# Optimization experiments

Measured on AMD Instinct MI355X. Metric: run time of the kernel, lower is better.

The kernel has to match this reference:

```python
import jax, jax.numpy as jnp
import numpy as np

B, C, Himg, Wimg = 8, 256, 128, 128
KC, VC, HID = 256, 256, 1024


def _conv(x, w, b, pad, groups=1):
    y = jax.lax.conv_general_dilated(
        x, w, (1, 1), [(pad[0], pad[0]), (pad[1], pad[1])],
        dimension_numbers=('NCHW', 'OIHW', 'NCHW'), feature_group_count=groups)
    return y + b[None, :, None, None]


def _ln(x, g, b, eps=1e-5):
    m = x.mean(-1, keepdims=True)
    v = ((x - m) ** 2).mean(-1, keepdims=True)
    return (x - m) / jnp.sqrt(v + eps) * g + b


def setup_inputs() -> dict:
    key = jax.random.key(0)
    ks = jax.random.split(key, 24)
    s = 0.02
    inp = {
        'x': jax.random.normal(ks[0], (B, C, Himg, Wimg), jnp.float32),
        'H': Himg, 'W': Wimg,
        # directional K/Q convs: dir0 kernel (1,3), dir1 kernel (3,1)
        'wk1': s * jax.random.normal(ks[1], (KC, C, 1, 3), jnp.float32),
        'bk1': jnp.zeros((KC,), jnp.float32),
        'wk2': s * jax.random.normal(ks[2], (KC, C, 3, 1), jnp.float32),
        'bk2': jnp.zeros((KC,), jnp.float32),
        'wq1': s * jax.random.normal(ks[3], (KC, C, 1, 3), jnp.float32),
        'bq1': jnp.zeros((KC,), jnp.float32),
        'wq2': s * jax.random.normal(ks[4], (KC, C, 3, 1), jnp.float32),
        'bq2': jnp.zeros((KC,), jnp.float32),
        'wv': s * jax.random.normal(ks[5], (VC, C, 1, 1), jnp.float32),
        'bv': jnp.zeros((VC,), jnp.float32),
        'wr': s * jax.random.normal(ks[6], (C, 2 * VC, 1, 1), jnp.float32),
        'br': jnp.zeros((C,), jnp.float32),
        'g1': jnp.ones((C,), jnp.float32), 'b1': jnp.zeros((C,), jnp.float32),
        'g2': jnp.ones((C,), jnp.float32), 'b2': jnp.zeros((C,), jnp.float32),
        'w_fc1': s * jax.random.normal(ks[7], (HID, C), jnp.float32),
        'b_fc1': jnp.zeros((HID,), jnp.float32),
        'w_dw': s * jax.random.normal(ks[8], (HID, 1, 3, 3), jnp.float32),
        'b_dw': jnp.zeros((HID,), jnp.float32),
        'w_fc2': s * jax.random.normal(ks[9], (C, HID), jnp.float32),
        'b_fc2': jnp.zeros((C,), jnp.float32),
    }
    return inp


def reference(x, H, W, wk1, bk1, wk2, bk2, wq1, bq1, wq2, bq2, wv, bv, wr, br,
              g1, b1, g2, b2, w_fc1, b_fc1, w_dw, b_dw, w_fc2, b_fc2):
    b, c, h, w = x.shape
    N = h * w
    xseq = x.reshape(b, c, N).transpose(0, 2, 1)          # b N c
    n1 = _ln(xseq, g1, b1)
    xn = n1.transpose(0, 2, 1).reshape(b, c, h, w)

    val = _conv(xn, wv, bv, (0, 0)).reshape(b, VC, N)     # b vc n
    attended, maps = [], []
    ctx = None
    for (wk, bk, wq, bq, pad) in [(wk1, bk1, wq1, bq1, (0, 1)),
                                  (wk2, bk2, wq2, bq2, (1, 0))]:
        k = _conv(xn, wk, bk, pad).reshape(b, KC, N)
        q = _conv(xn, wq, bq, pad).reshape(b, KC, N)
        key_s = jax.nn.softmax(k, axis=2)                 # softmax over spatial
        qry_s = jax.nn.softmax(q, axis=1)                 # softmax over channels
        ctx = jnp.einsum('bkn,bvn->bkv', key_s, val)      # O(n) linear attention
        av = jnp.einsum('bkv,bkn->bvn', ctx, qry_s).reshape(b, VC, h, w)
        attended.append(av)
        maps.append(key_s.mean(axis=1).reshape(b, h, w))
    agg = jnp.concatenate(attended, axis=1)               # b 2vc h w
    attn = _conv(agg, wr, br, (0, 0))                     # b c h w
    amap = jnp.stack(maps, axis=0).mean(axis=0)

    tx = xseq + attn.reshape(b, c, N).transpose(0, 2, 1)  # residual
    n2 = _ln(tx, g2, b2)
    h1 = n2 @ w_fc1.T + b_fc1                             # b N 4c
    h1img = h1.transpose(0, 2, 1).reshape(b, HID, h, w)
    dw = _conv(h1img, w_dw, b_dw, (1, 1), groups=HID)
    a = jax.nn.gelu(dw.reshape(b, HID, N).transpose(0, 2, 1), approximate=False)
    ffn = a @ w_fc2.T + b_fc2
    mx = (tx + ffn).transpose(0, 2, 1).reshape(b, c, h, w)
    return (mx, ctx, amap)
```

## Files before the change

### kernel.cpp

```cpp
#include <hip/hip_runtime.h>
#include <hip/hip_bf16.h>

#define B_ 8
#define C_ 256
#define H_ 128
#define W_ 128
#define N_ 16384
#define KC_ 256
#define VC_ 256
#define HID_ 1024

typedef unsigned short ushort_t;
typedef __bf16 bf16x8 __attribute__((ext_vector_type(8)));
typedef float f32x4 __attribute__((ext_vector_type(4)));
typedef ushort_t u16x8 __attribute__((ext_vector_type(8)));

static __device__ __forceinline__ ushort_t f2bu(float f) {
  __hip_bfloat16 h = __float2bfloat16(f);
  return *reinterpret_cast<ushort_t*>(&h);
}
static __device__ __forceinline__ float bu2f(ushort_t u) {
  __hip_bfloat16 h;
  *reinterpret_cast<ushort_t*>(&h) = u;
  return __bfloat162float(h);
}

#define GLD16(gp, lp) __builtin_amdgcn_global_load_lds( \
    (const __attribute__((address_space(1))) void*)(gp), \
    (__attribute__((address_space(3))) void*)(lp), 16, 0, 0)

__global__ __launch_bounds__(256) void pack_all(
    const float* __restrict__ wk1, const float* __restrict__ wk2,
    const float* __restrict__ wq1, const float* __restrict__ wq2,
    const float* __restrict__ wv, const float* __restrict__ wfc1,
    const float* __restrict__ wfc2, const float* __restrict__ wdw,
    const float* __restrict__ bk1, const float* __restrict__ bk2,
    const float* __restrict__ bq1, const float* __restrict__ bq2,
    const float* __restrict__ bv, const float* __restrict__ wr,
    ushort_t* __restrict__ zbuf,
    float* __restrict__ bKV, float* __restrict__ bQ, float* __restrict__ wdwT,
    ushort_t* __restrict__ wvp, ushort_t* __restrict__ wfc1p,
    ushort_t* __restrict__ wfc2p, ushort_t* __restrict__ wrp,
    ushort_t* __restrict__ wkkp, ushort_t* __restrict__ wqqp) {
  int idx = blockIdx.x * 256 + threadIdx.x;
  const int MC = KC_ * C_;
  if (idx < 512) {
    zbuf[idx] = 0;
    bQ[idx] = (idx < 256) ? bq1[idx] : bq2[idx - 256];
    return;
  }
  idx -= 512;
  if (idx < 768) {
    bKV[idx] = (idx < 256) ? bk1[idx] : (idx < 512 ? bk2[idx - 256] : bv[idx - 512]);
    return;
  }
  idx -= 768;
  if (idx < 9216) { int c = idx / 9, t = idx % 9; wdwT[t * HID_ + c] = wdw[idx]; return; }
  idx -= 9216;
  if (idx < VC_ * C_) { wvp[idx] = f2bu(wv[idx]); return; }
  idx -= VC_ * C_;
  if (idx < HID_ * C_) { wfc1p[idx] = f2bu(wfc1[idx]); return; }
  idx -= HID_ * C_;
  if (idx < C_ * HID_) { wfc2p[idx] = f2bu(wfc2[idx]); return; }
  idx -= C_ * HID_;
  if (idx < C_ * 512) { wrp[idx] = f2bu(wr[idx]); return; }
  idx -= C_ * 512;
  if (idx < MC) {
    #pragma unroll
    for (int t = 0; t < 3; ++t) wkkp[t * MC + idx] = f2bu(wk1[idx * 3 + t]);
    return;
  }
  idx -= MC;
  if (idx < MC) {
    #pragma unroll
    for (int t = 0; t < 3; ++t) wkkp[3 * MC + t * MC + idx] = f2bu(wk2[idx * 3 + t]);
    return;
  }
  idx -= MC;
  if (idx < MC) {
    #pragma unroll
    for (int t = 0; t < 3; ++t) wqqp[t * MC + idx] = f2bu(wq1[idx * 3 + t]);
    return;
  }
  idx -= MC;
  if (idx < MC) {
    #pragma unroll
    for (int t = 0; t < 3; ++t) wqqp[3 * MC + t * MC + idx] = f2bu(wq2[idx * 3 + t]);
    return;
  }
}

__global__ __launch_bounds__(256) void ln1t_kernel(const float* __restrict__ x,
    const float* __restrict__ g, const float* __restrict__ beta,
    ushort_t* __restrict__ out) {
  __shared__ float T[256][67];
  __shared__ float st[2][4][64];
  __shared__ float mr[64], rs[64];
  int z = blockIdx.z;
  int n0 = blockIdx.x * 64;
  int t = threadIdx.x;
  const float* xb = x + (size_t)z * C_ * N_;
  #pragma unroll
  for (int j = 0; j < 16; ++j) {
    int e = (j * 256 + t) * 4;
    int c = e >> 6, n = e & 63;
    float4 v = *(const float4*)&xb[(size_t)c * N_ + n0 + n];
    T[c][n] = v.x; T[c][n + 1] = v.y; T[c][n + 2] = v.z; T[c][n + 3] = v.w;
  }
  __syncthreads();
  {
    int n = t & 63, part = t >> 6;
    float s1 = 0.f, s2 = 0.f;
    for (int c = part * 64; c < part * 64 + 64; ++c) { float v = T[c][n]; s1 += v; s2 += v * v; }
    st[0][part][n] = s1; st[1][part][n] = s2;
  }
  __syncthreads();
  if (t < 64) {
    float s1 = st[0][0][t] + st[0][1][t] + st[0][2][t] + st[0][3][t];
    float s2 = st[1][0][t] + st[1][1][t] + st[1][2][t] + st[1][3][t];
    float m = s1 * (1.f / C_);
    float v = s2 * (1.f / C_) - m * m;
    mr[t] = m; rs[t] = rsqrtf(v + 1e-5f);
  }
  __syncthreads();
  {
    int n = t >> 2, cc = (t & 3) * 64;
    float m = mr[n], r = rs[n];
    ushort_t* po = out + (size_t)z * N_ * C_ + (size_t)(n0 + n) * C_ + cc;
    #pragma unroll
    for (int j0 = 0; j0 < 64; j0 += 8) {
      u16x8 o;
      #pragma unroll
      for (int j = 0; j < 8; ++j) {
        int c = cc + j0 + j;
        o[j] = f2bu((T[c][n] - m) * r * g[c] + beta[c]);
      }
      *(u16x8*)(po + j0) = o;
    }
  }
}

__global__ __launch_bounds__(256) void ln2t_kernel(const ushort_t* __restrict__ x,
    const float* __restrict__ g, const float* __restrict__ beta,
    ushort_t* __restrict__ out) {
  __shared__ ushort_t T[256][72];
  __shared__ float st[2][4][64];
  __shared__ float mr[64], rs[64];
  int z = blockIdx.z;
  int n0 = blockIdx.x * 64;
  int t = threadIdx.x;
  const ushort_t* xb = x + (size_t)z * C_ * N_;
  #pragma unroll
  for (int j = 0; j < 8; ++j) {
    int e = (j * 256 + t) * 8;
    int c = e >> 6, n = e & 63;
    *(u16x8*)&T[c][n] = *(const u16x8*)&xb[(size_t)c * N_ + n0 + n];
  }
  __syncthreads();
  {
    int n = t & 63, part = t >> 6;
    float s1 = 0.f, s2 = 0.f;
    for (int c = part * 64; c < part * 64 + 64; ++c) { float v = bu2f(T[c][n]); s1 += v; s2 += v * v; }
    st[0][part][n] = s1; st[1][part][n] = s2;
  }
  __syncthreads();
  if (t < 64) {
    float s1 = st[0][0][t] + st[0][1][t] + st[0][2][t] + st[0][3][t];
    float s2 = st[1][0][t] + st[1][1][t] + st[1][2][t] + st[1][3][t];
    float m = s1 * (1.f / C_);
    float v = s2 * (1.f / C_) - m * m;
    mr[t] = m; rs[t] = rsqrtf(v + 1e-5f);
  }
  __syncthreads();
  {
    int n = t >> 2, cc = (t & 3) * 64;
    float m = mr[n], r = rs[n];
    ushort_t* po = out + (size_t)z * N_ * C_ + (size_t)(n0 + n) * C_ + cc;
    #pragma unroll
    for (int j0 = 0; j0 < 64; j0 += 8) {
      u16x8 o;
      #pragma unroll
      for (int j = 0; j < 8; ++j) {
        int c = cc + j0 + j;
        o[j] = f2bu((bu2f(T[c][n]) - m) * r * g[c] + beta[c]);
      }
      *(u16x8*)(po + j0) = o;
    }
  }
}

template<int TAPS, int DIMSEL, int OMODE, int SPLIT, bool BDUAL>
__global__ __launch_bounds__(256) void mfma_gemm(
    const ushort_t* __restrict__ A, long Abatch, int lda, long Aplane, long Adirstride,
    const ushort_t* __restrict__ B, const ushort_t* __restrict__ B2, long Bbatch, int ldb,
    const float* __restrict__ bias,
    const float* __restrict__ resF, const ushort_t* __restrict__ resB, long Resbatch,
    float* __restrict__ outF, ushort_t* __restrict__ outB, ushort_t* __restrict__ outB2,
    ushort_t* __restrict__ outB3,
    long Outbatch, int ldo, int Ksteps, const ushort_t* __restrict__ zbuf) {
  __shared__ ushort_t sm[17408];
  int tid = threadIdx.x;
  int bx = blockIdx.x, by = blockIdx.y, bz = blockIdx.z;
  if (gridDim.x == 128) bx = ((bx & 7) << 4) | (bx >> 3);
  int b = bz / SPLIT, sK = bz % SPLIT;
  long koff = (long)sK * Ksteps * 64;
  int dsel = (DIMSEL == 3) ? (by < 2 ? 1 : 2)
           : (DIMSEL == 4) ? (by < 2 ? 1 : (by < 4 ? 2 : 0))
           : DIMSEL;
  int m0 = (DIMSEL == 3 || DIMSEL == 4) ? ((by & 1) * 128) : (by * 128);
  int bofs = (DIMSEL == 3 || DIMSEL == 4) ? ((by >> 1) * 256) : 0;
  const ushort_t* Ab = A + (size_t)b * Abatch + koff
      + ((DIMSEL == 3 || DIMSEL == 4) ? (long)(by >> 1) * Adirstride : 0L);
  const ushort_t* Bb = B + (size_t)b * Bbatch + (BDUAL ? 0 : koff);
  const ushort_t* B2b = BDUAL ? (B2 + (size_t)b * Bbatch) : nullptr;
  int n0 = bx * 128;
  int lane = tid & 63, wid = tid >> 6, wm = wid >> 1, wn = wid & 1;

  f32x4 acc[4][4];
  #pragma unroll
  for (int i = 0; i < 4; i++)
    #pragma unroll
    for (int j = 0; j < 4; j++) acc[i][j] = (f32x4)0.f;

  for (int t = 0; t < TAPS; ++t) {
    if (TAPS == 3 && dsel == 2) {
      if ((bx == 0 && t == 0) || (bx == H_ - 1 && t == 2)) continue;
    }
    if (DIMSEL == 4 && dsel == 0 && t != 1) continue;
    const ushort_t* At = Ab + ((DIMSEL == 4 && dsel == 0) ? 0L : (long)t * Aplane);
    for (int ks = 0; ks < Ksteps; ++ks) {
      int k0 = ks * 64;
      #pragma unroll
      for (int i = 0; i < 4; i++) {
        int s = tid + i * 256;
        int row = s >> 3, pc = s & 7;
        int lc = pc ^ (row & 7);
        const ushort_t* g = At + (long)(m0 + row) * lda + k0 + lc * 8;
        GLD16(g, &sm[s * 8]);
      }
      #pragma unroll
      for (int i = 0; i < 4; i++) {
        int s = tid + i * 256;
        int row = s >> 3, pc = s & 7;
        int lc = pc ^ (row & 7);
        const ushort_t* g;
        if (BDUAL) {
          const ushort_t* Bsel = (ks < Ksteps / 2) ? Bb : B2b;
          int kb = ((ks < Ksteps / 2) ? ks : ks - Ksteps / 2) * 64;
          g = Bsel + (long)(n0 + row) * ldb + kb + lc * 8;
        } else if (TAPS == 3 && dsel == 1) {
          int wpos = row + (t - 1);
          if (0 <= wpos && wpos < W_)
            g = Bb + (long)(n0 + row + (t - 1)) * ldb + k0 + lc * 8;
          else
            g = zbuf;
        } else if (TAPS == 3 && dsel == 2) {
          g = Bb + (long)(n0 + row + (t - 1) * W_) * ldb + k0 + lc * 8;
        } else {
          g = Bb + (long)(n0 + row) * ldb + k0 + lc * 8;
        }
        GLD16(g, &sm[8192 + s * 8]);
      }
      __syncthreads();
      #pragma unroll
      for (int kk = 0; kk < 2; kk++) {
        bf16x8 av[4], bv[4];
        int r16 = lane & 15;
        int sl = (lane >> 4) + kk * 4;
        #pragma unroll
        for (int fm = 0; fm < 4; fm++) {
          int row = wm * 64 + fm * 16 + r16;
          av[fm] = *(const bf16x8*)&sm[row * 64 + ((sl ^ (row & 7)) * 8)];
        }
        #pragma unroll
        for (int fn = 0; fn < 4; fn++) {
          int row = wn * 64 + fn * 16 + r16;
          bv[fn] = *(const bf16x8*)&sm[8192 + row * 64 + ((sl ^ (row & 7)) * 8)];
        }
        #pragma unroll
        for (int fm = 0; fm < 4; fm++)
          #pragma unroll
          for (int fn = 0; fn < 4; fn++)
            acc[fm][fn] = __builtin_amdgcn_mfma_f32_16x16x32_bf16(av[fm], bv[fn], acc[fm][fn], 0, 0, 0);
      }
      __syncthreads();
    }
  }

  int r16 = lane & 15, rq = lane >> 4;
  if (OMODE == 1 || OMODE == 2 || OMODE == 7) {
    ushort_t* obase;
    if (DIMSEL == 3 || DIMSEL == 4)
      obase = (blockIdx.y >= 4) ? outB3 : (blockIdx.y >= 2 ? outB2 : outB);
    else
      obase = outB;
    ushort_t* ob = obase + (size_t)bz * Outbatch;
    #pragma unroll
    for (int fm = 0; fm < 4; fm++) {
      #pragma unroll
      for (int fn = 0; fn < 4; fn++) {
        int lm = wm * 64 + fm * 16 + rq * 4;
        int ln = wn * 64 + fn * 16 + r16;
        f32x4 a = acc[fm][fn];
        if (OMODE == 2) {
          #pragma unroll
          for (int r = 0; r < 4; r++)
            sm[ln * 136 + lm + r] = f2bu(a[r] + bias[bofs + m0 + lm + r]);
        } else {
          #pragma unroll
          for (int r = 0; r < 4; r++)
            sm[(lm + r) * 136 + ln] = f2bu(a[r] + bias[bofs + m0 + lm + r]);
        }
      }
    }
    __syncthreads();
    int row = tid >> 1, half = (tid & 1) * 64;
    const ushort_t* src = &sm[row * 136 + half];
    if (OMODE == 7) {
      const float* xb = resF + (size_t)bz * Resbatch + (size_t)(m0 + row) * ldo + n0 + half;
      ushort_t* dst = &ob[(size_t)(m0 + row) * ldo + n0 + half];
      #pragma unroll
      for (int j = 0; j < 8; j++) {
        u16x8 v = *(const u16x8*)(src + j * 8);
        float4 x0 = *(const float4*)(xb + j * 8);
        float4 x1 = *(const float4*)(xb + j * 8 + 4);
        u16x8 o;
        o[0] = f2bu(bu2f(v[0]) + x0.x); o[1] = f2bu(bu2f(v[1]) + x0.y);
        o[2] = f2bu(bu2f(v[2]) + x0.z); o[3] = f2bu(bu2f(v[3]) + x0.w);
        o[4] = f2bu(bu2f(v[4]) + x1.x); o[5] = f2bu(bu2f(v[5]) + x1.y);
        o[6] = f2bu(bu2f(v[6]) + x1.z); o[7] = f2bu(bu2f(v[7]) + x1.w);
        *(u16x8*)(dst + j * 8) = o;
      }
    } else {
      ushort_t* dst;
      if (OMODE == 1) dst = &ob[(size_t)(m0 + row) * ldo + n0 + half];
      else            dst = &ob[(size_t)(n0 + row) * ldo + m0 + half];
      #pragma unroll
      for (int j = 0; j < 8; j++)
        *(u16x8*)(dst + j * 8) = *(const u16x8*)(src + j * 8);
    }
  } else {
    #pragma unroll
    for (int fm = 0; fm < 4; fm++) {
      #pragma unroll
      for (int fn = 0; fn < 4; fn++) {
        int mrow = m0 + wm * 64 + fm * 16 + rq * 4;
        int ncol = n0 + wn * 64 + fn * 16 + r16;
        f32x4 a = acc[fm][fn];
        if (OMODE == 6) {
          float* of = outF + (size_t)bz * Outbatch;
          #pragma unroll
          for (int r = 0; r < 4; r++)
            of[(size_t)(mrow + r) * ldo + ncol] = a[r];
        } else if (OMODE == 8) {
          float* of = outF + (size_t)bz * Outbatch;
          const ushort_t* rp = resB + (size_t)bz * Resbatch;
          #pragma unroll
          for (int r = 0; r < 4; r++) {
            size_t o = (size_t)(mrow + r) * ldo + ncol;
            of[o] = a[r] + bias[mrow + r] + bu2f(rp[o]);
          }
        }
      }
    }
  }
}

__global__ __launch_bounds__(256) void softmax_spatial2(ushort_t* __restrict__ p0,
                                                        ushort_t* __restrict__ p1) {
  int r = blockIdx.x;
  ushort_t* p = (r < B_ * KC_) ? (p0 + (size_t)r * N_) : (p1 + (size_t)(r - B_ * KC_) * N_);
  int tid = threadIdx.x;
  __shared__ float red[256];
  u16x8 v[8];
  #pragma unroll
  for (int j = 0; j < 8; j++) v[j] = *(const u16x8*)&p[tid * 8 + j * 2048];
  float mx = -1e30f;
  #pragma unroll
  for (int j = 0; j < 8; j++)
    #pragma unroll
    for (int e = 0; e < 8; e++) mx = fmaxf(mx, bu2f(v[j][e]));
  red[tid] = mx; __syncthreads();
  for (int s = 128; s > 0; s >>= 1) { if (tid < s) red[tid] = fmaxf(red[tid], red[tid + s]); __syncthreads(); }
  mx = red[0]; __syncthreads();
  float sum = 0.f;
  #pragma unroll
  for (int j = 0; j < 8; j++)
    #pragma unroll
    for (int e = 0; e < 8; e++) sum += __expf(bu2f(v[j][e]) - mx);
  red[tid] = sum; __syncthreads();
  for (int s = 128; s > 0; s >>= 1) { if (tid < s) red[tid] += red[tid + s]; __syncthreads(); }
  float inv = 1.f / red[0];
  #pragma unroll
  for (int j = 0; j < 8; j++) {
    u16x8 o;
    #pragma unroll
    for (int e = 0; e < 8; e++) o[e] = f2bu(__expf(bu2f(v[j][e]) - mx) * inv);
    *(u16x8*)&p[tid * 8 + j * 2048] = o;
  }
}

__global__ __launch_bounds__(256) void softmax_channel2(ushort_t* __restrict__ p0,
                                                        ushort_t* __restrict__ p1) {
  int tid = threadIdx.x;
  size_t rowg = (size_t)blockIdx.x * 32 + (tid >> 3);
  int part = tid & 7;
  ushort_t* q = (rowg < (size_t)B_ * N_) ? (p0 + rowg * KC_)
                                         : (p1 + (rowg - (size_t)B_ * N_) * KC_);
  u16x8 v[4];
  #pragma unroll
  for (int j = 0; j < 4; j++) v[j] = *(const u16x8*)&q[part * 8 + j * 64];
  float mx = -1e30f;
  #pragma unroll
  for (int j = 0; j < 4; j++)
    #pragma unroll
    for (int e = 0; e < 8; e++) mx = fmaxf(mx, bu2f(v[j][e]));
  mx = fmaxf(mx, __shfl_xor(mx, 1));
  mx = fmaxf(mx, __shfl_xor(mx, 2));
  mx = fmaxf(mx, __shfl_xor(mx, 4));
  float sum = 0.f;
  #pragma unroll
  for (int j = 0; j < 4; j++)
    #pragma unroll
    for (int e = 0; e < 8; e++) sum += __expf(bu2f(v[j][e]) - mx);
  sum += __shfl_xor(sum, 1);
  sum += __shfl_xor(sum, 2);
  sum += __shfl_xor(sum, 4);
  float inv = 1.f / sum;
  #pragma unroll
  for (int j = 0; j < 4; j++) {
    u16x8 o;
    #pragma unroll
    for (int e = 0; e < 8; e++) o[e] = f2bu(__expf(bu2f(v[j][e]) - mx) * inv);
    *(u16x8*)&q[part * 8 + j * 64] = o;
  }
}

__global__ __launch_bounds__(256) void amap2_kernel(const ushort_t* __restrict__ k0,
    const ushort_t* __restrict__ k1, float* __restrict__ amap) {
  __shared__ float red[256][8];
  int tid = threadIdx.x;
  int ngrp = tid & 63, part = tid >> 6;
  int nblock = blockIdx.x * 512;
  int b = nblock >> 14;
  int n = (nblock & 16383) + ngrp * 8;
  const ushort_t* b0 = k0 + (size_t)b * KC_ * N_ + n;
  const ushort_t* b1 = k1 + (size_t)b * KC_ * N_ + n;
  float s[8];
  #pragma unroll
  for (int j = 0; j < 8; j++) s[j] = 0.f;
  for (int c = part * 64; c < part * 64 + 64; ++c) {
    u16x8 a = *(const u16x8*)&b0[(size_t)c * N_];
    u16x8 d = *(const u16x8*)&b1[(size_t)c * N_];
    #pragma unroll
    for (int j = 0; j < 8; j++) s[j] += bu2f(a[j]) + bu2f(d[j]);
  }
  #pragma unroll
  for (int j = 0; j < 8; j++) red[tid][j] = s[j];
  __syncthreads();
  if (tid < 64) {
    float t[8];
    #pragma unroll
    for (int j = 0; j < 8; j++)
      t[j] = (red[tid][j] + red[tid + 64][j] + red[tid + 128][j] + red[tid + 192][j])
             * (1.f / (2.f * KC_));
    float* dst = amap + (size_t)nblock + tid * 8;
    *(float4*)dst = make_float4(t[0], t[1], t[2], t[3]);
    *(float4*)(dst + 4) = make_float4(t[4], t[5], t[6], t[7]);
  }
}

template<bool F32OUT>
__global__ __launch_bounds__(256) void ctx_reduce(const float* __restrict__ part,
                                                  float* __restrict__ outF,
                                                  ushort_t* __restrict__ outB, int split) {
  int idx = blockIdx.x * 256 + threadIdx.x;
  int b = idx >> 16;
  int r = idx & 65535;
  float s = 0.f;
  for (int k = 0; k < split; k++)
    s += part[((size_t)(b * split + k)) * KC_ * VC_ + r];
  if (F32OUT) outF[idx] = s;
  outB[idx] = f2bu(s);
}

__global__ __launch_bounds__(256) void dwgelu_t(const ushort_t* __restrict__ h1t,
    const float* __restrict__ wdwT, const float* __restrict__ bdw,
    ushort_t* __restrict__ actT) {
  int pix = blockIdx.x * 2 + (threadIdx.x >> 7);
  int c = (threadIdx.x & 127) * 8;
  int h = pix >> 7, w = pix & 127;
  float s[8];
  {
    float4 b0 = *(const float4*)&bdw[c];
    float4 b1 = *(const float4*)&bdw[c + 4];
    s[0]=b0.x; s[1]=b0.y; s[2]=b0.z; s[3]=b0.w;
    s[4]=b1.x; s[5]=b1.y; s[6]=b1.z; s[7]=b1.w;
  }
  #pragma unroll
  for (int di = -1; di <= 1; ++di) {
    int h2 = h + di;
    if ((unsigned)h2 >= H_) continue;
    #pragma unroll
    for (int dj = -1; dj <= 1; ++dj) {
      int w2 = w + dj;
      if ((unsigned)w2 >= W_) continue;
      int tap = (di + 1) * 3 + (dj + 1);
      u16x8 v = *(const u16x8*)&h1t[(size_t)(h2 * W_ + w2) * HID_ + c];
      const float* wp = &wdwT[tap * HID_ + c];
      float4 w0 = *(const float4*)wp, w1 = *(const float4*)(wp + 4);
      s[0] += w0.x * bu2f(v[0]); s[1] += w0.y * bu2f(v[1]);
      s[2] += w0.z * bu2f(v[2]); s[3] += w0.w * bu2f(v[3]);
      s[4] += w1.x * bu2f(v[4]); s[5] += w1.y * bu2f(v[5]);
      s[6] += w1.z * bu2f(v[6]); s[7] += w1.w * bu2f(v[7]);
    }
  }
  u16x8 o;
  #pragma unroll
  for (int j = 0; j < 8; j++) {
    float gl = 0.5f * s[j] * (1.f + erff(s[j] * 0.70710678118654752f));
    o[j] = f2bu(gl);
  }
  *(u16x8*)&actT[(size_t)pix * HID_ + c] = o;
}

extern "C" void kernel_launch(void* const* d_in, const int* in_sizes, int n_in,
                              void* d_out, int out_size, void* d_ws, size_t ws_size,
                              hipStream_t stream) {
  const float* x    = (const float*)d_in[0];
  const float* wk1  = (const float*)d_in[3];
  const float* bk1  = (const float*)d_in[4];
  const float* wk2  = (const float*)d_in[5];
  const float* bk2  = (const float*)d_in[6];
  const float* wq1  = (const float*)d_in[7];
  const float* bq1  = (const float*)d_in[8];
  const float* wq2  = (const float*)d_in[9];
  const float* bq2  = (const float*)d_in[10];
  const float* wv   = (const float*)d_in[11];
  const float* bv   = (const float*)d_in[12];
  const float* wr   = (const float*)d_in[13];
  const float* br   = (const float*)d_in[14];
  const float* g1   = (const float*)d_in[15];
  const float* b1   = (const float*)d_in[16];
  const float* g2   = (const float*)d_in[17];
  const float* b2   = (const float*)d_in[18];
  const float* wfc1 = (const float*)d_in[19];
  const float* bfc1 = (const float*)d_in[20];
  const float* wdw  = (const float*)d_in[21];
  const float* bdw  = (const float*)d_in[22];
  const float* wfc2 = (const float*)d_in[23];
  const float* bfc2 = (const float*)d_in[24];

  const size_t big = (size_t)B_ * C_ * N_;
  const long  CN  = (long)C_ * N_;
  const long  NC2 = (long)N_ * C_;
  const int   MC  = KC_ * C_;

  uint8_t* w8 = (uint8_t*)d_ws;
  size_t off = 0;
  ushort_t* xnt  = (ushort_t*)(w8 + off); off += 67108864;
  ushort_t* kq   = (ushort_t*)(w8 + off); off += 67108864;
  ushort_t* Mbuf = (ushort_t*)(w8 + off); off += (size_t)B_ * C_ * 512 * 2;
  ushort_t* wkkp = (ushort_t*)(w8 + off); off += 6 * MC * 2;
  ushort_t* wvp  = (ushort_t*)(w8 + off); off += MC * 2;
  ushort_t* wqqp = (ushort_t*)(w8 + off); off += 6 * MC * 2;
  ushort_t* wfc1p= (ushort_t*)(w8 + off); off += HID_ * C_ * 2;
  ushort_t* wfc2p= (ushort_t*)(w8 + off); off += C_ * HID_ * 2;
  float* wdwT    = (float*)(w8 + off);    off += 9 * HID_ * 4;
  float* bKV     = (float*)(w8 + off);    off += 768 * 4;
  float* bQ      = (float*)(w8 + off);    off += 512 * 4;
  ushort_t* wrp  = (ushort_t*)(w8 + off); off += C_ * 512 * 2;
  ushort_t* ctx0b= (ushort_t*)(w8 + off); off += (size_t)B_ * KC_ * VC_ * 2;
  ushort_t* ctx1b= (ushort_t*)(w8 + off); off += (size_t)B_ * KC_ * VC_ * 2;
  ushort_t* zbuf = (ushort_t*)(w8 + off); off += 1024;
  float* part    = (float*)(w8 + off);
  size_t need4 = off + (size_t)4 * B_ * KC_ * VC_ * 4;
  size_t need8 = off + (size_t)8 * B_ * KC_ * VC_ * 4;
  int csplit;
  if (ws_size >= need8) csplit = 8;
  else if (ws_size >= need4) csplit = 4;
  else return;
  const float* fzero = (const float*)zbuf;

  float* mx_out   = (float*)d_out;
  float* ctx_out  = mx_out + big;
  float* amap_out = ctx_out + (size_t)B_ * KC_ * VC_;

  ushort_t* mxlo = (ushort_t*)d_out;
  ushort_t* mxhi = (ushort_t*)d_out + big;

  ushort_t* txn  = xnt;
  ushort_t* h1t  = kq;
  ushort_t* actT = kq + (size_t)N_ * HID_;

  dim3 blk(256);

  pack_all<<<3881, blk, 0, stream>>>(wk1, wk2, wq1, wq2, wv, wfc1, wfc2, wdw,
                                     bk1, bk2, bq1, bq2, bv, wr,
                                     zbuf, bKV, bQ, wdwT,
                                     wvp, wfc1p, wfc2p, wrp, wkkp, wqqp);

  ln1t_kernel<<<dim3(N_ / 64, 1, B_), blk, 0, stream>>>(x, g1, b1, xnt);

  mfma_gemm<3, 4, 1, 1, false><<<dim3(N_ / 128, 6, B_), blk, 0, stream>>>(
      wkkp, 0, C_, (long)MC, (long)3 * MC, xnt, nullptr, NC2, C_,
      bKV, nullptr, nullptr, 0,
      nullptr, kq, mxhi, mxlo, (long)KC_ * N_, N_, C_ / 64, zbuf);

  softmax_spatial2<<<2 * B_ * KC_, blk, 0, stream>>>(kq, mxhi);
  amap2_kernel<<<B_ * N_ / 512, blk, 0, stream>>>(kq, mxhi, amap_out);

  for (int d = 0; d < 2; ++d) {
    const ushort_t* Ksrc = d ? mxhi : kq;
    if (csplit == 8)
      mfma_gemm<1, 0, 6, 8, false><<<dim3(VC_ / 128, KC_ / 128, B_ * 8), blk, 0, stream>>>(
          Ksrc, (long)KC_ * N_, N_, 0, 0, mxlo, nullptr, (long)VC_ * N_, N_,
          nullptr, nullptr, nullptr, 0,
          part, nullptr, nullptr, nullptr, (long)KC_ * VC_, VC_, (N_ / 8) / 64, zbuf);
    else
      mfma_gemm<1, 0, 6, 4, false><<<dim3(VC_ / 128, KC_ / 128, B_ * 4), blk, 0, stream>>>(
          Ksrc, (long)KC_ * N_, N_, 0, 0, mxlo, nullptr, (long)VC_ * N_, N_,
          nullptr, nullptr, nullptr, 0,
          part, nullptr, nullptr, nullptr, (long)KC_ * VC_, VC_, (N_ / 4) / 64, zbuf);
    if (d == 0)
      ctx_reduce<false><<<B_ * KC_ * VC_ / 256, blk, 0, stream>>>(part, nullptr, ctx0b, csplit);
    else
      ctx_reduce<true><<<B_ * KC_ * VC_ / 256, blk, 0, stream>>>(part, ctx_out, ctx1b, csplit);
  }

  mfma_gemm<3, 3, 2, 1, false><<<dim3(N_ / 128, 4, B_), blk, 0, stream>>>(
      wqqp, 0, C_, (long)MC, (long)3 * MC, xnt, nullptr, NC2, C_,
      bQ, nullptr, nullptr, 0,
      nullptr, kq, mxlo, nullptr, (long)N_ * KC_, KC_, C_ / 64, zbuf);

  softmax_channel2<<<2 * B_ * N_ / 32, blk, 0, stream>>>(kq, mxlo);

  mfma_gemm<1, 0, 1, 1, false><<<dim3(KC_ / 128, C_ / 128, B_), blk, 0, stream>>>(
      wrp, 0, 512, 0, 0, ctx0b, nullptr, (long)KC_ * VC_, VC_, fzero, nullptr, nullptr, 0,
      nullptr, Mbuf, nullptr, nullptr, (long)C_ * 512, 512, VC_ / 64, zbuf);
  mfma_gemm<1, 0, 1, 1, false><<<dim3(KC_ / 128, C_ / 128, B_), blk, 0, stream>>>(
      wrp + 256, 0, 512, 0, 0, ctx1b, nullptr, (long)KC_ * VC_, VC_, fzero, nullptr, nullptr, 0,
      nullptr, Mbuf + 256, nullptr, nullptr, (long)C_ * 512, 512, VC_ / 64, zbuf);

  mfma_gemm<1, 0, 7, 1, true><<<dim3(N_ / 128, C_ / 128, B_), blk, 0, stream>>>(
      Mbuf, (long)C_ * 512, 512, 0, 0, kq, mxlo, (long)N_ * KC_, KC_,
      br, x, nullptr, CN,
      nullptr, mxhi, nullptr, nullptr, CN, N_, 8, zbuf);

  ln2t_kernel<<<dim3(N_ / 64, 1, B_), blk, 0, stream>>>(mxhi, g2, b2, txn);

  hipMemcpyAsync(part, mxhi + (size_t)7 * CN, (size_t)CN * 2,
                 hipMemcpyDeviceToDevice, stream);

  for (int b = 0; b < B_; ++b) {
    mfma_gemm<1, 0, 2, 1, false><<<dim3(N_ / 128, HID_ / 128, 1), blk, 0, stream>>>(
        wfc1p, 0, C_, 0, 0, txn + (size_t)b * NC2, nullptr, 0, C_,
        bfc1, nullptr, nullptr, 0,
        nullptr, h1t, nullptr, nullptr, 0, HID_, C_ / 64, zbuf);
    dwgelu_t<<<N_ / 2, blk, 0, stream>>>(h1t, wdwT, bdw, actT);
    const ushort_t* txb = (b == 7) ? (const ushort_t*)part : (mxhi + (size_t)b * CN);
    mfma_gemm<1, 0, 8, 1, false><<<dim3(N_ / 128, C_ / 128, 1), blk, 0, stream>>>(
        wfc2p, 0, HID_, 0, 0, actT, nullptr, 0, HID_,
        bfc2, nullptr, txb, 0,
        mx_out + (size_t)b * CN, nullptr, nullptr, nullptr, 0, N_, HID_ / 64, zbuf);
  }
}
```

Measured before the change: 1.437 ms.

## Fuse channel softmax into the output GEMM loader and batch FFN in pairs

The channel softmax pass no longer rewrites the query tensor. A stats kernel stores a per-row max and inverse sum, and the residual GEMM applies exp-normalize while staging B tiles into shared memory. This removes one full read-write pass over the Q tensors, but the B loads become synchronous register loads with extra exp work instead of direct async copies. Separately, when the workspace is large enough, the FFN runs two batches per launch using an extra 64MB activation buffer, halving the launch count and doubling grid size for the FFN kernels.

```diff
diff --git a/kernel.cpp b/kernel.cpp
--- a/kernel.cpp
+++ b/kernel.cpp
@@ -189,7 +189,7 @@
   }
 }
 
-template<int TAPS, int DIMSEL, int OMODE, int SPLIT, bool BDUAL>
+template<int TAPS, int DIMSEL, int OMODE, int SPLIT, bool BDUAL, bool BSOFT>
 __global__ __launch_bounds__(256) void mfma_gemm(
     const ushort_t* __restrict__ A, long Abatch, int lda, long Aplane, long Adirstride,
     const ushort_t* __restrict__ B, const ushort_t* __restrict__ B2, long Bbatch, int ldb,
@@ -197,7 +197,8 @@
     const float* __restrict__ resF, const ushort_t* __restrict__ resB, long Resbatch,
     float* __restrict__ outF, ushort_t* __restrict__ outB, ushort_t* __restrict__ outB2,
     ushort_t* __restrict__ outB3,
-    long Outbatch, int ldo, int Ksteps, const ushort_t* __restrict__ zbuf) {
+    long Outbatch, int ldo, int Ksteps, const ushort_t* __restrict__ zbuf,
+    const float2* __restrict__ qstats) {
   __shared__ ushort_t sm[17408];
   int tid = threadIdx.x;
   int bx = blockIdx.x, by = blockIdx.y, bz = blockIdx.z;
@@ -238,28 +239,47 @@
         const ushort_t* g = At + (long)(m0 + row) * lda + k0 + lc * 8;
         GLD16(g, &sm[s * 8]);
       }
-      #pragma unroll
-      for (int i = 0; i < 4; i++) {
-        int s = tid + i * 256;
-        int row = s >> 3, pc = s & 7;
-        int lc = pc ^ (row & 7);
-        const ushort_t* g;
-        if (BDUAL) {
-          const ushort_t* Bsel = (ks < Ksteps / 2) ? Bb : B2b;
-          int kb = ((ks < Ksteps / 2) ? ks : ks - Ksteps / 2) * 64;
-          g = Bsel + (long)(n0 + row) * ldb + kb + lc * 8;
-        } else if (TAPS == 3 && dsel == 1) {
-          int wpos = row + (t - 1);
-          if (0 <= wpos && wpos < W_)
-            g = Bb + (long)(n0 + row + (t - 1)) * ldb + k0 + lc * 8;
-          else
-            g = zbuf;
-        } else if (TAPS == 3 && dsel == 2) {
-          g = Bb + (long)(n0 + row + (t - 1) * W_) * ldb + k0 + lc * 8;
-        } else {
-          g = Bb + (long)(n0 + row) * ldb + k0 + lc * 8;
+      if (BDUAL && BSOFT) {
+        int dir = (ks < Ksteps / 2) ? 0 : 1;
+        const ushort_t* Bsel = dir ? B2b : Bb;
+        int kb = (ks - dir * (Ksteps / 2)) * 64;
+        #pragma unroll
+        for (int i = 0; i < 4; i++) {
+          int s = tid + i * 256;
+          int row = s >> 3, pc = s & 7;
+          int lc = pc ^ (row & 7);
+          u16x8 e = *(const u16x8*)(Bsel + (long)(n0 + row) * ldb + kb + lc * 8);
+          float2 st = qstats[(size_t)dir * B_ * N_ + (size_t)bz * N_ + n0 + row];
+          u16x8 o;
+          #pragma unroll
+          for (int j = 0; j < 8; j++)
+            o[j] = f2bu(__expf(bu2f(e[j]) - st.x) * st.y);
+          *(u16x8*)&sm[8192 + s * 8] = o;
         }
-        GLD16(g, &sm[8192 + s * 8]);
+      } else {
+        #pragma unroll
+        for (int i = 0; i < 4; i++) {
+          int s = tid + i * 256;
+          int row = s >> 3, pc = s & 7;
+          int lc = pc ^ (row & 7);
+          const ushort_t* g;
+          if (BDUAL) {
+            const ushort_t* Bsel = (ks < Ksteps / 2) ? Bb : B2b;
+            int kb = ((ks < Ksteps / 2) ? ks : ks - Ksteps / 2) * 64;
+            g = Bsel + (long)(n0 + row) * ldb + kb + lc * 8;
+          } else if (TAPS == 3 && dsel == 1) {
+            int wpos = row + (t - 1);
+            if (0 <= wpos && wpos < W_)
+              g = Bb + (long)(n0 + row + (t - 1)) * ldb + k0 + lc * 8;
+            else
+              g = zbuf;
+          } else if (TAPS == 3 && dsel == 2) {
+            g = Bb + (long)(n0 + row + (t - 1) * W_) * ldb + k0 + lc * 8;
+          } else {
+            g = Bb + (long)(n0 + row) * ldb + k0 + lc * 8;
+          }
+          GLD16(g, &sm[8192 + s * 8]);
+        }
       }
       __syncthreads();
       #pragma unroll
@@ -400,13 +420,14 @@
   }
 }
 
-__global__ __launch_bounds__(256) void softmax_channel2(ushort_t* __restrict__ p0,
-                                                        ushort_t* __restrict__ p1) {
+__global__ __launch_bounds__(256) void chstats_kernel(const ushort_t* __restrict__ p0,
+                                                      const ushort_t* __restrict__ p1,
+                                                      float2* __restrict__ qstats) {
   int tid = threadIdx.x;
   size_t rowg = (size_t)blockIdx.x * 32 + (tid >> 3);
   int part = tid & 7;
-  ushort_t* q = (rowg < (size_t)B_ * N_) ? (p0 + rowg * KC_)
-                                         : (p1 + (rowg - (size_t)B_ * N_) * KC_);
+  const ushort_t* q = (rowg < (size_t)B_ * N_) ? (p0 + rowg * KC_)
+                                               : (p1 + (rowg - (size_t)B_ * N_) * KC_);
   u16x8 v[4];
   #pragma unroll
   for (int j = 0; j < 4; j++) v[j] = *(const u16x8*)&q[part * 8 + j * 64];
@@ -426,14 +447,7 @@
   sum += __shfl_xor(sum, 1);
   sum += __shfl_xor(sum, 2);
   sum += __shfl_xor(sum, 4);
-  float inv = 1.f / sum;
-  #pragma unroll
-  for (int j = 0; j < 4; j++) {
-    u16x8 o;
-    #pragma unroll
-    for (int e = 0; e < 8; e++) o[e] = f2bu(__expf(bu2f(v[j][e]) - mx) * inv);
-    *(u16x8*)&q[part * 8 + j * 64] = o;
-  }
+  if (part == 0) qstats[rowg] = make_float2(mx, 1.f / sum);
 }
 
 __global__ __launch_bounds__(256) void amap2_kernel(const ushort_t* __restrict__ k0,
@@ -487,6 +501,8 @@
 __global__ __launch_bounds__(256) void dwgelu_t(const ushort_t* __restrict__ h1t,
     const float* __restrict__ wdwT, const float* __restrict__ bdw,
     ushort_t* __restrict__ actT) {
+  const ushort_t* h1 = h1t + (size_t)blockIdx.y * N_ * HID_;
+  ushort_t* act = actT + (size_t)blockIdx.y * N_ * HID_;
   int pix = blockIdx.x * 2 + (threadIdx.x >> 7);
   int c = (threadIdx.x & 127) * 8;
   int h = pix >> 7, w = pix & 127;
@@ -506,7 +522,7 @@
       int w2 = w + dj;
       if ((unsigned)w2 >= W_) continue;
       int tap = (di + 1) * 3 + (dj + 1);
-      u16x8 v = *(const u16x8*)&h1t[(size_t)(h2 * W_ + w2) * HID_ + c];
+      u16x8 v = *(const u16x8*)&h1[(size_t)(h2 * W_ + w2) * HID_ + c];
       const float* wp = &wdwT[tap * HID_ + c];
       float4 w0 = *(const float4*)wp, w1 = *(const float4*)(wp + 4);
       s[0] += w0.x * bu2f(v[0]); s[1] += w0.y * bu2f(v[1]);
@@ -521,7 +537,7 @@
     float gl = 0.5f * s[j] * (1.f + erff(s[j] * 0.70710678118654752f));
     o[j] = f2bu(gl);
   }
-  *(u16x8*)&actT[(size_t)pix * HID_ + c] = o;
+  *(u16x8*)&act[(size_t)pix * HID_ + c] = o;
 }
 
 extern "C" void kernel_launch(void* const* d_in, const int* in_sizes, int n_in,
@@ -554,6 +570,7 @@
   const size_t big = (size_t)B_ * C_ * N_;
   const long  CN  = (long)C_ * N_;
   const long  NC2 = (long)N_ * C_;
+  const long  NH  = (long)N_ * HID_;
   const int   MC  = KC_ * C_;
 
   uint8_t* w8 = (uint8_t*)d_ws;
@@ -572,14 +589,24 @@
   ushort_t* wrp  = (ushort_t*)(w8 + off); off += C_ * 512 * 2;
   ushort_t* ctx0b= (ushort_t*)(w8 + off); off += (size_t)B_ * KC_ * VC_ * 2;
   ushort_t* ctx1b= (ushort_t*)(w8 + off); off += (size_t)B_ * KC_ * VC_ * 2;
+  float2* qstats = (float2*)(w8 + off);   off += (size_t)2 * B_ * N_ * 8;
   ushort_t* zbuf = (ushort_t*)(w8 + off); off += 1024;
-  float* part    = (float*)(w8 + off);
-  size_t need4 = off + (size_t)4 * B_ * KC_ * VC_ * 4;
-  size_t need8 = off + (size_t)8 * B_ * KC_ * VC_ * 4;
-  int csplit;
-  if (ws_size >= need8) csplit = 8;
-  else if (ws_size >= need4) csplit = 4;
-  else return;
+  const size_t partBytes = (size_t)8 * B_ * KC_ * VC_ * 4;
+  size_t need_pair = off + 67108864 + partBytes;
+  size_t need8 = off + partBytes;
+  size_t need4 = off + partBytes / 2;
+  int csplit; bool pairFFN = false;
+  ushort_t* actX = nullptr;
+  float* part;
+  if (ws_size >= need_pair) {
+    pairFFN = true; csplit = 8;
+    actX = (ushort_t*)(w8 + off);
+    part = (float*)(w8 + off + 67108864);
+  } else if (ws_size >= need8) {
+    csplit = 8; part = (float*)(w8 + off);
+  } else if (ws_size >= need4) {
+    csplit = 4; part = (float*)(w8 + off);
+  } else return;
   const float* fzero = (const float*)zbuf;
 
   float* mx_out   = (float*)d_out;
@@ -590,8 +617,6 @@
   ushort_t* mxhi = (ushort_t*)d_out + big;
 
   ushort_t* txn  = xnt;
-  ushort_t* h1t  = kq;
-  ushort_t* actT = kq + (size_t)N_ * HID_;
 
   dim3 blk(256);
 
@@ -602,10 +627,10 @@
 
   ln1t_kernel<<<dim3(N_ / 64, 1, B_), blk, 0, stream>>>(x, g1, b1, xnt);
 
-  mfma_gemm<3, 4, 1, 1, false><<<dim3(N_ / 128, 6, B_), blk, 0, stream>>>(
+  mfma_gemm<3, 4, 1, 1, false, false><<<dim3(N_ / 128, 6, B_), blk, 0, stream>>>(
       wkkp, 0, C_, (long)MC, (long)3 * MC, xnt, nullptr, NC2, C_,
       bKV, nullptr, nullptr, 0,
-      nullptr, kq, mxhi, mxlo, (long)KC_ * N_, N_, C_ / 64, zbuf);
+      nullptr, kq, mxhi, mxlo, (long)KC_ * N_, N_, C_ / 64, zbuf, nullptr);
 
   softmax_spatial2<<<2 * B_ * KC_, blk, 0, stream>>>(kq, mxhi);
   amap2_kernel<<<B_ * N_ / 512, blk, 0, stream>>>(kq, mxhi, amap_out);
@@ -613,55 +638,74 @@
   for (int d = 0; d < 2; ++d) {
     const ushort_t* Ksrc = d ? mxhi : kq;
     if (csplit == 8)
-      mfma_gemm<1, 0, 6, 8, false><<<dim3(VC_ / 128, KC_ / 128, B_ * 8), blk, 0, stream>>>(
+      mfma_gemm<1, 0, 6, 8, false, false><<<dim3(VC_ / 128, KC_ / 128, B_ * 8), blk, 0, stream>>>(
           Ksrc, (long)KC_ * N_, N_, 0, 0, mxlo, nullptr, (long)VC_ * N_, N_,
           nullptr, nullptr, nullptr, 0,
-          part, nullptr, nullptr, nullptr, (long)KC_ * VC_, VC_, (N_ / 8) / 64, zbuf);
+          part, nullptr, nullptr, nullptr, (long)KC_ * VC_, VC_, (N_ / 8) / 64, zbuf, nullptr);
     else
-      mfma_gemm<1, 0, 6, 4, false><<<dim3(VC_ / 128, KC_ / 128, B_ * 4), blk, 0, stream>>>(
+      mfma_gemm<1, 0, 6, 4, false, false><<<dim3(VC_ / 128, KC_ / 128, B_ * 4), blk, 0, stream>>>(
           Ksrc, (long)KC_ * N_, N_, 0, 0, mxlo, nullptr, (long)VC_ * N_, N_,
           nullptr, nullptr, nullptr, 0,
-          part, nullptr, nullptr, nullptr, (long)KC_ * VC_, VC_, (N_ / 4) / 64, zbuf);
+          part, nullptr, nullptr, nullptr, (long)KC_ * VC_, VC_, (N_ / 4) / 64, zbuf, nullptr);
     if (d == 0)
       ctx_reduce<false><<<B_ * KC_ * VC_ / 256, blk, 0, stream>>>(part, nullptr, ctx0b, csplit);
     else
       ctx_reduce<true><<<B_ * KC_ * VC_ / 256, blk, 0, stream>>>(part, ctx_out, ctx1b, csplit);
   }
 
-  mfma_gemm<3, 3, 2, 1, false><<<dim3(N_ / 128, 4, B_), blk, 0, stream>>>(
+  mfma_gemm<3, 3, 2, 1, false, false><<<dim3(N_ / 128, 4, B_), blk, 0, stream>>>(
       wqqp, 0, C_, (long)MC, (long)3 * MC, xnt, nullptr, NC2, C_,
       bQ, nullptr, nullptr, 0,
-      nullptr, kq, mxlo, nullptr, (long)N_ * KC_, KC_, C_ / 64, zbuf);
-
-  softmax_channel2<<<2 * B_ * N_ / 32, blk, 0, stream>>>(kq, mxlo);
-
-  mfma_gemm<1, 0, 1, 1, false><<<dim3(KC_ / 128, C_ / 128, B_), blk, 0, stream>>>(
+      nullptr, kq, mxlo, nullptr, (long)N_ * KC_, KC_, C_ / 64, zbuf, nullptr);
+
+  chstats_kernel<<<2 * B_ * N_ / 32, blk, 0, stream>>>(kq, mxlo, qstats);
+
+  mfma_gemm<1, 0, 1, 1, false, false><<<dim3(KC_ / 128, C_ / 128, B_), blk, 0, stream>>>(
       wrp, 0, 512, 0, 0, ctx0b, nullptr, (long)KC_ * VC_, VC_, fzero, nullptr, nullptr, 0,
-      nullptr, Mbuf, nullptr, nullptr, (long)C_ * 512, 512, VC_ / 64, zbuf);
-  mfma_gemm<1, 0, 1, 1, false><<<dim3(KC_ / 128, C_ / 128, B_), blk, 0, stream>>>(
+      nullptr, Mbuf, nullptr, nullptr, (long)C_ * 512, 512, VC_ / 64, zbuf, nullptr);
+  mfma_gemm<1, 0, 1, 1, false, false><<<dim3(KC_ / 128, C_ / 128, B_), blk, 0, stream>>>(
       wrp + 256, 0, 512, 0, 0, ctx1b, nullptr, (long)KC_ * VC_, VC_, fzero, nullptr, nullptr, 0,
-      nullptr, Mbuf + 256, nullptr, nullptr, (long)C_ * 512, 512, VC_ / 64, zbuf);
-
-  mfma_gemm<1, 0, 7, 1, true><<<dim3(N_ / 128, C_ / 128, B_), blk, 0, stream>>>(
+      nullptr, Mbuf + 256, nullptr, nullptr, (long)C_ * 512, 512, VC_ / 64, zbuf, nullptr);
+
+  mfma_gemm<1, 0, 7, 1, true, true><<<dim3(N_ / 128, C_ / 128, B_), blk, 0, stream>>>(
       Mbuf, (long)C_ * 512, 512, 0, 0, kq, mxlo, (long)N_ * KC_, KC_,
       br, x, nullptr, CN,
-      nullptr, mxhi, nullptr, nullptr, CN, N_, 8, zbuf);
+      nullptr, mxhi, nullptr, nullptr, CN, N_, 8, zbuf, qstats);
 
   ln2t_kernel<<<dim3(N_ / 64, 1, B_), blk, 0, stream>>>(mxhi, g2, b2, txn);
 
-  hipMemcpyAsync(part, mxhi + (size_t)7 * CN, (size_t)CN * 2,
-                 hipMemcpyDeviceToDevice, stream);
-
-  for (int b = 0; b < B_; ++b) {
-    mfma_gemm<1, 0, 2, 1, false><<<dim3(N_ / 128, HID_ / 128, 1), blk, 0, stream>>>(
-        wfc1p, 0, C_, 0, 0, txn + (size_t)b * NC2, nullptr, 0, C_,
-        bfc1, nullptr, nullptr, 0,
-        nullptr, h1t, nullptr, nullptr, 0, HID_, C_ / 64, zbuf);
-    dwgelu_t<<<N_ / 2, blk, 0, stream>>>(h1t, wdwT, bdw, actT);
-    const ushort_t* txb = (b == 7) ? (const ushort_t*)part : (mxhi + (size_t)b * CN);
-    mfma_gemm<1, 0, 8, 1, false><<<dim3(N_ / 128, C_ / 128, 1), blk, 0, stream>>>(
-        wfc2p, 0, HID_, 0, 0, actT, nullptr, 0, HID_,
-        bfc2, nullptr, txb, 0,
-        mx_out + (size_t)b * CN, nullptr, nullptr, nullptr, 0, N_, HID_ / 64, zbuf);
-  }
-}
+  if (pairFFN) {
+    hipMemcpyAsync(part, mxhi + (size_t)6 * CN, (size_t)2 * CN * 2,
+                   hipMemcpyDeviceToDevice, stream);
+    ushort_t* h1t2 = kq;
+    for (int g = 0; g < 4; ++g) {
+      mfma_gemm<1, 0, 2, 1, false, false><<<dim3(N_ / 128, HID_ / 128, 2), blk, 0, stream>>>(
+          wfc1p, 0, C_, 0, 0, txn + (size_t)g * 2 * NC2, nullptr, NC2, C_,
+          bfc1, nullptr, nullptr, 0,
+          nullptr, h1t2, nullptr, nullptr, NH, HID_, C_ / 64, zbuf, nullptr);
+      dwgelu_t<<<dim3(N_ / 2, 2), blk, 0, stream>>>(h1t2, wdwT, bdw, actX);
+      const ushort_t* txb = (g == 3) ? (const ushort_t*)part : (mxhi + (size_t)g * 2 * CN);
+      mfma_gemm<1, 0, 8, 1, false, false><<<dim3(N_ / 128, C_ / 128, 2), blk, 0, stream>>>(
+          wfc2p, 0, HID_, 0, 0, actX, nullptr, NH, HID_,
+          bfc2, nullptr, txb, CN,
+          mx_out + (size_t)g * 2 * CN, nullptr, nullptr, nullptr, CN, N_, HID_ / 64, zbuf, nullptr);
+    }
+  } else {
+    ushort_t* h1t  = kq;
+    ushort_t* actT = kq + NH;
+    hipMemcpyAsync(part, mxhi + (size_t)7 * CN, (size_t)CN * 2,
+                   hipMemcpyDeviceToDevice, stream);
+    for (int b = 0; b < B_; ++b) {
+      mfma_gemm<1, 0, 2, 1, false, false><<<dim3(N_ / 128, HID_ / 128, 1), blk, 0, stream>>>(
+          wfc1p, 0, C_, 0, 0, txn + (size_t)b * NC2, nullptr, 0, C_,
+          bfc1, nullptr, nullptr, 0,
+          nullptr, h1t, nullptr, nullptr, 0, HID_, C_ / 64, zbuf, nullptr);
+      dwgelu_t<<<dim3(N_ / 2, 1), blk, 0, stream>>>(h1t, wdwT, bdw, actT);
+      const ushort_t* txb = (b == 7) ? (const ushort_t*)part : (mxhi + (size_t)b * CN);
+      mfma_gemm<1, 0, 8, 1, false, false><<<dim3(N_ / 128, C_ / 128, 1), blk, 0, stream>>>(
+          wfc2p, 0, HID_, 0, 0, actT, nullptr, 0, HID_,
+          bfc2, nullptr, txb, 0,
+          mx_out + (size_t)b * CN, nullptr, nullptr, nullptr, 0, N_, HID_ / 64, zbuf, nullptr);
+    }
+  }
+}
```

Result: faster. 1.334 ms (-7.2%).
